# Kernel tuning notes

Hardware: AMD Instinct MI355X
Metric: run time of the kernel (lower is better)

Reference implementation:

```python
import jax, jax.numpy as jnp
import numpy as np

MARGIN = 0.3


def _l2norm(x, axis=-1):
    return x / (jnp.linalg.norm(x, axis=axis, keepdims=True) + 1e-12)


def setup_inputs() -> dict:
    key = jax.random.key(0)
    k1, k2, k3, k4 = jax.random.split(key, 4)
    n, P, d = 1024, 8, 2048
    global_feat = jax.random.normal(k1, (n, d), dtype=jnp.float32)
    partial_feat = jax.random.normal(k2, (n, P, d), dtype=jnp.float32)
    part_labels = jax.random.randint(k3, (n, P), 0, 2).astype(jnp.float32)
    global_labels = jax.random.randint(k4, (n,), 0, 64).astype(jnp.int64)
    return {"global_feat": global_feat, "partial_feat": partial_feat,
            "part_labels": part_labels, "global_labels": global_labels}


def reference(global_feat, partial_feat, part_labels, global_labels):
    # --- compute_distance (VGTripletLoss) ---
    g = _l2norm(global_feat)            # [n, d]
    p = _l2norm(partial_feat)           # [n, P, d]
    gs = (1.0 - g @ g.T) / 2.0          # [n, n]
    overlap = part_labels[:, None, :] * part_labels[None, :, :]   # [n, n, P]
    # per-part cosine distance: [n, n, P]
    slf = (1.0 - jnp.einsum('ipd,jpd->ijp', p, p)) / 2.0
    slf = slf * overlap
    dist = (slf.sum(-1) + gs) / (overlap.sum(-1) + 1.0)            # [n, n]

    # --- compute_loss: hard positive/negative mining ---
    mask = global_labels[:, None] == global_labels[None, :]        # [n, n]
    neg_inf = jnp.float32(-1e30)
    pos_inf = jnp.float32(1e30)
    dist_ap = jnp.max(jnp.where(mask, dist, neg_inf), axis=1)      # hardest positive
    dist_an = jnp.min(jnp.where(mask, pos_inf, dist), axis=1)      # hardest negative
    # MarginRankingLoss(y=1, reduction='mean'): max(0, dist_ap - dist_an + margin)
    loss = jnp.mean(jax.nn.relu(dist_ap - dist_an + MARGIN))
    return loss
```

## Files before the change

### kernel.cpp

```cpp
#include <hip/hip_runtime.h>

#define N 1024
#define D 2048
#define P 8
#define F 9
#define KTOT (F * D)
#define BM 128
#define BKT 32
#define MARGIN 0.3f

typedef float f32x4 __attribute__((ext_vector_type(4)));
typedef short s16x8 __attribute__((ext_vector_type(8)));

#define GLOBAL_AS __attribute__((address_space(1)))
#define LDS_AS __attribute__((address_space(3)))

__device__ __forceinline__ const float* feat_row(const float* __restrict__ g,
                                                 const float* __restrict__ p,
                                                 int i, int f) {
    return (f == 0) ? (g + (size_t)i * D)
                    : (p + ((size_t)i * P + (f - 1)) * D);
}

__device__ __forceinline__ unsigned f2bf(float x) {
    unsigned u = __float_as_uint(x);
    return (u + 0x7fffu + ((u >> 16) & 1u)) >> 16;
}

__global__ __launch_bounds__(256)
void pack_kernel(const float* __restrict__ gfeat,
                 const float* __restrict__ pfeat,
                 const float* __restrict__ plab,
                 unsigned short* __restrict__ V) {
    const int wid = (blockIdx.x << 2) | (threadIdx.x >> 6);
    const int lane = threadIdx.x & 63;
    const int i = wid / F, f = wid % F;
    const float* src = feat_row(gfeat, pfeat, i, f);
    const float4* s4 = (const float4*)src;
    float4 a[4][2];
    #pragma unroll
    for (int q = 0; q < 4; ++q) {
        a[q][0] = s4[(q * 64 + lane) * 2];
        a[q][1] = s4[(q * 64 + lane) * 2 + 1];
    }
    float ss = 0.f;
    #pragma unroll
    for (int q = 0; q < 4; ++q)
        #pragma unroll
        for (int h = 0; h < 2; ++h)
            ss += a[q][h].x * a[q][h].x + a[q][h].y * a[q][h].y
                + a[q][h].z * a[q][h].z + a[q][h].w * a[q][h].w;
    #pragma unroll
    for (int m = 32; m > 0; m >>= 1) ss += __shfl_xor(ss, m, 64);
    const float ls = (f == 0) ? 1.0f : plab[i * P + (f - 1)];
    const float inv = ls / (sqrtf(ss) + 1e-12f);
    unsigned short* dst = V + (size_t)wid * D;
    #pragma unroll
    for (int q = 0; q < 4; ++q) {
        uint4 o;
        o.x = f2bf(a[q][0].x * inv) | (f2bf(a[q][0].y * inv) << 16);
        o.y = f2bf(a[q][0].z * inv) | (f2bf(a[q][0].w * inv) << 16);
        o.z = f2bf(a[q][1].x * inv) | (f2bf(a[q][1].y * inv) << 16);
        o.w = f2bf(a[q][1].z * inv) | (f2bf(a[q][1].w * inv) << 16);
        *(uint4*)&dst[(size_t)(q * 64 + lane) * 8] = o;
    }
}

__global__ __launch_bounds__(256)
void gemm_kernel(const unsigned short* __restrict__ V,
                 float* __restrict__ part, int ks) {
    __shared__ short As[2][BM * BKT];
    __shared__ short Bs[2][BM * BKT];

    const int nwg = gridDim.x * gridDim.y;
    const int l = blockIdx.x + gridDim.x * blockIdx.y;
    const int q = nwg >> 3;
    const int wg = (l & 7) * q + (l >> 3);
    const int t36 = wg % 36;
    const int bz = wg / 36;

    int by = 0, rem = t36;
    while (rem >= 8 - by) { rem -= 8 - by; ++by; }
    const int bx = by + rem;

    const int t = threadIdx.x;
    const int wave = t >> 6, lane = t & 63;
    const int i0 = by * BM;
    const int j0 = bx * BM;
    const int kbase = bz * ks;
    const int nsteps = ks >> 5;

    const unsigned short* Ap = V + (size_t)(i0 + (t >> 2)) * KTOT + kbase + (t & 3) * 8;
    const unsigned short* Bp = V + (size_t)(j0 + (t >> 2)) * KTOT + kbase + (t & 3) * 8;

    const int kq = lane >> 4;
    const int aoff = ((wave & 1) * 64 + (lane & 15)) * BKT + kq * 8;
    const int boff = ((wave >> 1) * 64 + (lane & 15)) * BKT + kq * 8;

    f32x4 acc[4][4];
    #pragma unroll
    for (int m = 0; m < 4; ++m)
        #pragma unroll
        for (int n = 0; n < 4; ++n)
            acc[m][n] = (f32x4){0.f, 0.f, 0.f, 0.f};

#define STAGE(b) do {                                                          \
    __builtin_amdgcn_global_load_lds((const GLOBAL_AS void*)Ap,                \
        (LDS_AS void*)(&As[(b)][0] + t * 8), 16, 0, 0);                        \
    __builtin_amdgcn_global_load_lds((const GLOBAL_AS void*)(Ap + (size_t)64 * KTOT), \
        (LDS_AS void*)(&As[(b)][2048] + t * 8), 16, 0, 0);                     \
    __builtin_amdgcn_global_load_lds((const GLOBAL_AS void*)Bp,                \
        (LDS_AS void*)(&Bs[(b)][0] + t * 8), 16, 0, 0);                        \
    __builtin_amdgcn_global_load_lds((const GLOBAL_AS void*)(Bp + (size_t)64 * KTOT), \
        (LDS_AS void*)(&Bs[(b)][2048] + t * 8), 16, 0, 0);                     \
    Ap += BKT; Bp += BKT;                                                      \
} while (0)

#define COMPUTE(b) do {                                                        \
    s16x8 af[4], bf[4];                                                        \
    _Pragma("unroll")                                                          \
    for (int m = 0; m < 4; ++m)                                                \
        af[m] = *(const s16x8*)(&As[(b)][aoff + m * 16 * BKT]);                \
    _Pragma("unroll")                                                          \
    for (int n = 0; n < 4; ++n)                                                \
        bf[n] = *(const s16x8*)(&Bs[(b)][boff + n * 16 * BKT]);                \
    _Pragma("unroll")                                                          \
    for (int m = 0; m < 4; ++m)                                                \
        _Pragma("unroll")                                                      \
        for (int n = 0; n < 4; ++n)                                            \
            acc[m][n] = __builtin_amdgcn_mfma_f32_16x16x32_bf16(               \
                af[m], bf[n], acc[m][n], 0, 0, 0);                             \
} while (0)

    STAGE(0);
    __syncthreads();

    int cur = 0;
    for (int ksi = 0; ksi < nsteps - 1; ++ksi) {
        STAGE(cur ^ 1);
        COMPUTE(cur);
        __syncthreads();
        cur ^= 1;
    }
    COMPUTE(cur);

#undef STAGE
#undef COMPUTE

    float* outp = part + (size_t)bz * N * N;
    const int rbase = i0 + (wave & 1) * 64 + (lane >> 4) * 4;
    const int cbase = j0 + (wave >> 1) * 64 + (lane & 15);
    #pragma unroll
    for (int m = 0; m < 4; ++m)
        #pragma unroll
        for (int n = 0; n < 4; ++n)
            #pragma unroll
            for (int r = 0; r < 4; ++r)
                outp[(size_t)(rbase + m * 16 + r) * N + cbase + n * 16] = acc[m][n][r];

    if (bx != by) {
        #pragma unroll
        for (int m = 0; m < 4; ++m)
            #pragma unroll
            for (int n = 0; n < 4; ++n)
                #pragma unroll
                for (int r = 0; r < 4; ++r)
                    outp[(size_t)(cbase + n * 16) * N + rbase + m * 16 + r] = acc[m][n][r];
    }
}

template <int S>
__global__ __launch_bounds__(256)
void mine_kernel(const float* __restrict__ part,
                 const float* __restrict__ plab,
                 const int* __restrict__ glab,
                 float* __restrict__ rowloss) {
    const int i = blockIdx.x;
    const int t = threadIdx.x;
    const int wave = t >> 6, lane = t & 63;
    const int j = t * 4;

    float4 dot = {0.f, 0.f, 0.f, 0.f};
    #pragma unroll
    for (int s = 0; s < S; ++s) {
        float4 v = *(const float4*)&part[(size_t)s * N * N + (size_t)i * N + j];
        dot.x += v.x; dot.y += v.y; dot.z += v.z; dot.w += v.w;
    }

    float labj[4][8];
    const float4* pj = (const float4*)&plab[(size_t)j * P];
    #pragma unroll
    for (int q = 0; q < 8; ++q) ((float4*)labj)[q] = pj[q];
    int4 gj = *(const int4*)&glab[j];

    const int li = glab[i];
    float lab_i[P];
    #pragma unroll
    for (int c = 0; c < P; ++c) lab_i[c] = plab[i * P + c];

    float ap = -1e30f, an = 1e30f;
    const float dv[4] = {dot.x, dot.y, dot.z, dot.w};
    const int gv[4] = {gj.x, gj.y, gj.z, gj.w};
    #pragma unroll
    for (int u = 0; u < 4; ++u) {
        float ov = 0.f;
        #pragma unroll
        for (int c = 0; c < P; ++c) ov += lab_i[c] * labj[u][c];
        float d = 0.5f - dv[u] / (2.0f * (ov + 1.0f));
        if (gv[u] == li) ap = fmaxf(ap, d);
        else             an = fminf(an, d);
    }

    #pragma unroll
    for (int m = 32; m > 0; m >>= 1) {
        ap = fmaxf(ap, __shfl_xor(ap, m, 64));
        an = fminf(an, __shfl_xor(an, m, 64));
    }
    __shared__ float sap[4], san[4];
    if (lane == 0) { sap[wave] = ap; san[wave] = an; }
    __syncthreads();
    if (t == 0) {
        float A = fmaxf(fmaxf(sap[0], sap[1]), fmaxf(sap[2], sap[3]));
        float B = fminf(fminf(san[0], san[1]), fminf(san[2], san[3]));
        rowloss[i] = fmaxf(0.f, A - B + MARGIN);
    }
}

__global__ void reduce_kernel(const float* __restrict__ rowloss,
                              float* __restrict__ out) {
    const int t = threadIdx.x;
    float s = rowloss[t] + rowloss[t + 256] + rowloss[t + 512] + rowloss[t + 768];
    __shared__ float red[256];
    red[t] = s;
    __syncthreads();
    for (int st = 128; st > 0; st >>= 1) {
        if (t < st) red[t] += red[t + st];
        __syncthreads();
    }
    if (t == 0) out[0] = red[0] * (1.0f / N);
}

extern "C" void kernel_launch(void* const* d_in, const int* in_sizes, int n_in,
                              void* d_out, int out_size, void* d_ws, size_t ws_size,
                              hipStream_t stream) {
    const float* gfeat = (const float*)d_in[0];
    const float* pfeat = (const float*)d_in[1];
    const float* plab  = (const float*)d_in[2];
    const int*   glab  = (const int*)d_in[3];
    float* out = (float*)d_out;

    const size_t vbytes = (size_t)N * KTOT * 2;
    const size_t slice  = (size_t)N * N * 4;

    int S = (ws_size != 0 && ws_size >= vbytes + 16 * slice + 4096) ? 16 : 8;
    const int ks = KTOT / S;

    char* ws = (char*)d_ws;
    unsigned short* V = (unsigned short*)ws;
    float* part    = (float*)(ws + vbytes);
    float* rowloss = (float*)(ws + vbytes + (size_t)S * slice);

    pack_kernel<<<N * F / 4, 256, 0, stream>>>(gfeat, pfeat, plab, V);
    gemm_kernel<<<dim3(36, S), 256, 0, stream>>>(V, part, ks);
    if (S == 16)
        mine_kernel<16><<<N, 256, 0, stream>>>(part, plab, glab, rowloss);
    else
        mine_kernel<8><<<N, 256, 0, stream>>>(part, plab, glab, rowloss);
    reduce_kernel<<<1, 256, 0, stream>>>(rowloss, out);
}
```

Before: 164.4 us.

## Double GEMM K-tile with XOR-swizzled LDS layout and batch rows in mining kernel

The GEMM K-step grows from 32 to 64 bf16 elements, halving the number of barrier-separated iterations. The global-to-LDS staging is reorganised so each wave loads 8-row groups into an XOR-swizzled layout, and fragment reads apply the same swizzle to avoid LDS bank conflicts on the wider rows. LDS use per buffer doubles. The mining kernel now handles four rows per block, reusing the column-label loads and launching a quarter as many blocks, at the cost of extra barriers per row.

After: 170.7 us. 1.04x slower.

```diff
diff --git a/kernel.cpp b/kernel.cpp
--- a/kernel.cpp
+++ b/kernel.cpp
@@ -6,7 +6,7 @@
 #define F 9
 #define KTOT (F * D)
 #define BM 128
-#define BKT 32
+#define BKT 64
 #define MARGIN 0.3f
 
 typedef float f32x4 __attribute__((ext_vector_type(4)));
@@ -88,14 +88,19 @@
     const int i0 = by * BM;
     const int j0 = bx * BM;
     const int kbase = bz * ks;
-    const int nsteps = ks >> 5;
-
-    const unsigned short* Ap = V + (size_t)(i0 + (t >> 2)) * KTOT + kbase + (t & 3) * 8;
-    const unsigned short* Bp = V + (size_t)(j0 + (t >> 2)) * KTOT + kbase + (t & 3) * 8;
+    const int nsteps = ks >> 6;
+
+    const int sg = lane >> 3;
+    const int sc = lane & 7;
+    const int rl0 = wave * 32 + sg;
+    const unsigned short* Ag = V + (size_t)(i0 + rl0) * KTOT + kbase + ((sc ^ sg) << 3);
+    const unsigned short* Bg = V + (size_t)(j0 + rl0) * KTOT + kbase + ((sc ^ sg) << 3);
+    const int ldsoff = wave * 2048 + sg * 64 + sc * 8;
 
     const int kq = lane >> 4;
-    const int aoff = ((wave & 1) * 64 + (lane & 15)) * BKT + kq * 8;
-    const int boff = ((wave >> 1) * 64 + (lane & 15)) * BKT + kq * 8;
+    const int r7 = lane & 7;
+    const int arow0 = (wave & 1) * 64 + (lane & 15);
+    const int brow0 = (wave >> 1) * 64 + (lane & 15);
 
     f32x4 acc[4][4];
     #pragma unroll
@@ -105,31 +110,39 @@
             acc[m][n] = (f32x4){0.f, 0.f, 0.f, 0.f};
 
 #define STAGE(b) do {                                                          \
-    __builtin_amdgcn_global_load_lds((const GLOBAL_AS void*)Ap,                \
-        (LDS_AS void*)(&As[(b)][0] + t * 8), 16, 0, 0);                        \
-    __builtin_amdgcn_global_load_lds((const GLOBAL_AS void*)(Ap + (size_t)64 * KTOT), \
-        (LDS_AS void*)(&As[(b)][2048] + t * 8), 16, 0, 0);                     \
-    __builtin_amdgcn_global_load_lds((const GLOBAL_AS void*)Bp,                \
-        (LDS_AS void*)(&Bs[(b)][0] + t * 8), 16, 0, 0);                        \
-    __builtin_amdgcn_global_load_lds((const GLOBAL_AS void*)(Bp + (size_t)64 * KTOT), \
-        (LDS_AS void*)(&Bs[(b)][2048] + t * 8), 16, 0, 0);                     \
-    Ap += BKT; Bp += BKT;                                                      \
+    _Pragma("unroll")                                                          \
+    for (int c = 0; c < 4; ++c) {                                              \
+        __builtin_amdgcn_global_load_lds(                                      \
+            (const GLOBAL_AS void*)(Ag + (size_t)(c * 8) * KTOT),              \
+            (LDS_AS void*)(&As[(b)][ldsoff + c * 512]), 16, 0, 0);             \
+        __builtin_amdgcn_global_load_lds(                                      \
+            (const GLOBAL_AS void*)(Bg + (size_t)(c * 8) * KTOT),              \
+            (LDS_AS void*)(&Bs[(b)][ldsoff + c * 512]), 16, 0, 0);             \
+    }                                                                          \
+    Ag += BKT; Bg += BKT;                                                      \
 } while (0)
 
 #define COMPUTE(b) do {                                                        \
-    s16x8 af[4], bf[4];                                                        \
     _Pragma("unroll")                                                          \
-    for (int m = 0; m < 4; ++m)                                                \
-        af[m] = *(const s16x8*)(&As[(b)][aoff + m * 16 * BKT]);                \
-    _Pragma("unroll")                                                          \
-    for (int n = 0; n < 4; ++n)                                                \
-        bf[n] = *(const s16x8*)(&Bs[(b)][boff + n * 16 * BKT]);                \
-    _Pragma("unroll")                                                          \
-    for (int m = 0; m < 4; ++m)                                                \
+    for (int ks2 = 0; ks2 < 2; ++ks2) {                                        \
+        s16x8 af[4], bf[4];                                                    \
         _Pragma("unroll")                                                      \
-        for (int n = 0; n < 4; ++n)                                            \
-            acc[m][n] = __builtin_amdgcn_mfma_f32_16x16x32_bf16(               \
-                af[m], bf[n], acc[m][n], 0, 0, 0);                             \
+        for (int m = 0; m < 4; ++m) {                                          \
+            const int R = arow0 + m * 16;                                      \
+            af[m] = *(const s16x8*)(&As[(b)][R * 64 + (((ks2 * 4 + kq) ^ r7) * 8)]); \
+        }                                                                      \
+        _Pragma("unroll")                                                      \
+        for (int n = 0; n < 4; ++n) {                                          \
+            const int R = brow0 + n * 16;                                      \
+            bf[n] = *(const s16x8*)(&Bs[(b)][R * 64 + (((ks2 * 4 + kq) ^ r7) * 8)]); \
+        }                                                                      \
+        _Pragma("unroll")                                                      \
+        for (int m = 0; m < 4; ++m)                                            \
+            _Pragma("unroll")                                                  \
+            for (int n = 0; n < 4; ++n)                                        \
+                acc[m][n] = __builtin_amdgcn_mfma_f32_16x16x32_bf16(           \
+                    af[m], bf[n], acc[m][n], 0, 0, 0);                         \
+    }                                                                          \
 } while (0)
 
     STAGE(0);
@@ -175,54 +188,61 @@
                  const float* __restrict__ plab,
                  const int* __restrict__ glab,
                  float* __restrict__ rowloss) {
-    const int i = blockIdx.x;
+    const int i0 = blockIdx.x * 4;
     const int t = threadIdx.x;
     const int wave = t >> 6, lane = t & 63;
     const int j = t * 4;
 
-    float4 dot = {0.f, 0.f, 0.f, 0.f};
-    #pragma unroll
-    for (int s = 0; s < S; ++s) {
-        float4 v = *(const float4*)&part[(size_t)s * N * N + (size_t)i * N + j];
-        dot.x += v.x; dot.y += v.y; dot.z += v.z; dot.w += v.w;
-    }
-
     float labj[4][8];
     const float4* pj = (const float4*)&plab[(size_t)j * P];
     #pragma unroll
-    for (int q = 0; q < 8; ++q) ((float4*)labj)[q] = pj[q];
-    int4 gj = *(const int4*)&glab[j];
-
-    const int li = glab[i];
-    float lab_i[P];
-    #pragma unroll
-    for (int c = 0; c < P; ++c) lab_i[c] = plab[i * P + c];
-
-    float ap = -1e30f, an = 1e30f;
-    const float dv[4] = {dot.x, dot.y, dot.z, dot.w};
+    for (int qq = 0; qq < 8; ++qq) ((float4*)labj)[qq] = pj[qq];
+    const int4 gj = *(const int4*)&glab[j];
     const int gv[4] = {gj.x, gj.y, gj.z, gj.w};
-    #pragma unroll
-    for (int u = 0; u < 4; ++u) {
-        float ov = 0.f;
-        #pragma unroll
-        for (int c = 0; c < P; ++c) ov += lab_i[c] * labj[u][c];
-        float d = 0.5f - dv[u] / (2.0f * (ov + 1.0f));
-        if (gv[u] == li) ap = fmaxf(ap, d);
-        else             an = fminf(an, d);
-    }
-
-    #pragma unroll
-    for (int m = 32; m > 0; m >>= 1) {
-        ap = fmaxf(ap, __shfl_xor(ap, m, 64));
-        an = fminf(an, __shfl_xor(an, m, 64));
-    }
+
     __shared__ float sap[4], san[4];
-    if (lane == 0) { sap[wave] = ap; san[wave] = an; }
-    __syncthreads();
-    if (t == 0) {
-        float A = fmaxf(fmaxf(sap[0], sap[1]), fmaxf(sap[2], sap[3]));
-        float B = fminf(fminf(san[0], san[1]), fminf(san[2], san[3]));
-        rowloss[i] = fmaxf(0.f, A - B + MARGIN);
+
+    #pragma unroll
+    for (int ri = 0; ri < 4; ++ri) {
+        const int i = i0 + ri;
+
+        float4 dot = {0.f, 0.f, 0.f, 0.f};
+        #pragma unroll
+        for (int s = 0; s < S; ++s) {
+            float4 v = *(const float4*)&part[(size_t)s * N * N + (size_t)i * N + j];
+            dot.x += v.x; dot.y += v.y; dot.z += v.z; dot.w += v.w;
+        }
+
+        const int li = glab[i];
+        float lab_i[P];
+        #pragma unroll
+        for (int c = 0; c < P; ++c) lab_i[c] = plab[i * P + c];
+
+        float ap = -1e30f, an = 1e30f;
+        const float dv[4] = {dot.x, dot.y, dot.z, dot.w};
+        #pragma unroll
+        for (int u = 0; u < 4; ++u) {
+            float ov = 0.f;
+            #pragma unroll
+            for (int c = 0; c < P; ++c) ov += lab_i[c] * labj[u][c];
+            float d = 0.5f - dv[u] / (2.0f * (ov + 1.0f));
+            if (gv[u] == li) ap = fmaxf(ap, d);
+            else             an = fminf(an, d);
+        }
+
+        #pragma unroll
+        for (int m = 32; m > 0; m >>= 1) {
+            ap = fmaxf(ap, __shfl_xor(ap, m, 64));
+            an = fminf(an, __shfl_xor(an, m, 64));
+        }
+        if (lane == 0) { sap[wave] = ap; san[wave] = an; }
+        __syncthreads();
+        if (t == 0) {
+            float A = fmaxf(fmaxf(sap[0], sap[1]), fmaxf(sap[2], sap[3]));
+            float B = fminf(fminf(san[0], san[1]), fminf(san[2], san[3]));
+            rowloss[i] = fmaxf(0.f, A - B + MARGIN);
+        }
+        __syncthreads();
     }
 }
 
@@ -263,8 +283,8 @@
     pack_kernel<<<N * F / 4, 256, 0, stream>>>(gfeat, pfeat, plab, V);
     gemm_kernel<<<dim3(36, S), 256, 0, stream>>>(V, part, ks);
     if (S == 16)
-        mine_kernel<16><<<N, 256, 0, stream>>>(part, plab, glab, rowloss);
+        mine_kernel<16><<<N / 4, 256, 0, stream>>>(part, plab, glab, rowloss);
     else
-        mine_kernel<8><<<N, 256, 0, stream>>>(part, plab, glab, rowloss);
+        mine_kernel<8><<<N / 4, 256, 0, stream>>>(part, plab, glab, rowloss);
     reduce_kernel<<<1, 256, 0, stream>>>(rowloss, out);
 }
```

## Swizzle GEMM LDS layout, relax barriers with vmcnt waits, batch mining rows

Applied to the files above, without the earlier changes.

Applies an XOR swizzle to the k-chunk placement in LDS for both the staging writes and the MFMA fragment reads, to cut LDS bank conflicts. It also replaces __syncthreads with explicit s_waitcnt vmcnt plus s_barrier, so the next tile's async loads can stay in flight while the current tile computes. The mining kernel now handles 4 rows per block to reuse the column labels and cut the block count, at the cost of extra barriers per row. The hand-written waitcnt counts are fragile if the compiler reorders or adds memory operations.

Measured after the change: 164.1 us. Within noise of the previous version (-0.2%).

```diff
diff --git a/kernel.cpp b/kernel.cpp
--- a/kernel.cpp
+++ b/kernel.cpp
@@ -90,12 +90,16 @@
     const int kbase = bz * ks;
     const int nsteps = ks >> 5;
 
-    const unsigned short* Ap = V + (size_t)(i0 + (t >> 2)) * KTOT + kbase + (t & 3) * 8;
-    const unsigned short* Bp = V + (size_t)(j0 + (t >> 2)) * KTOT + kbase + (t & 3) * 8;
+    const int srow = t >> 2;
+    const int schunk = (t & 3) ^ ((t >> 3) & 3);
+    const unsigned short* Ag = V + (size_t)(i0 + srow) * KTOT + kbase + schunk * 8;
+    const unsigned short* Bg = V + (size_t)(j0 + srow) * KTOT + kbase + schunk * 8;
 
     const int kq = lane >> 4;
-    const int aoff = ((wave & 1) * 64 + (lane & 15)) * BKT + kq * 8;
-    const int boff = ((wave >> 1) * 64 + (lane & 15)) * BKT + kq * 8;
+    const int rsw = ((lane & 15) >> 1) & 3;
+    const int kk = (kq ^ rsw) * 8;
+    const int arow0 = (wave & 1) * 64 + (lane & 15);
+    const int brow0 = (wave >> 1) * 64 + (lane & 15);
 
     f32x4 acc[4][4];
     #pragma unroll
@@ -105,25 +109,25 @@
             acc[m][n] = (f32x4){0.f, 0.f, 0.f, 0.f};
 
 #define STAGE(b) do {                                                          \
-    __builtin_amdgcn_global_load_lds((const GLOBAL_AS void*)Ap,                \
-        (LDS_AS void*)(&As[(b)][0] + t * 8), 16, 0, 0);                        \
-    __builtin_amdgcn_global_load_lds((const GLOBAL_AS void*)(Ap + (size_t)64 * KTOT), \
-        (LDS_AS void*)(&As[(b)][2048] + t * 8), 16, 0, 0);                     \
-    __builtin_amdgcn_global_load_lds((const GLOBAL_AS void*)Bp,                \
-        (LDS_AS void*)(&Bs[(b)][0] + t * 8), 16, 0, 0);                        \
-    __builtin_amdgcn_global_load_lds((const GLOBAL_AS void*)(Bp + (size_t)64 * KTOT), \
-        (LDS_AS void*)(&Bs[(b)][2048] + t * 8), 16, 0, 0);                     \
-    Ap += BKT; Bp += BKT;                                                      \
+    __builtin_amdgcn_global_load_lds((const GLOBAL_AS void*)Ag,                \
+        (LDS_AS void*)(&As[(b)][t * 8]), 16, 0, 0);                            \
+    __builtin_amdgcn_global_load_lds((const GLOBAL_AS void*)(Ag + (size_t)64 * KTOT), \
+        (LDS_AS void*)(&As[(b)][2048 + t * 8]), 16, 0, 0);                     \
+    __builtin_amdgcn_global_load_lds((const GLOBAL_AS void*)Bg,                \
+        (LDS_AS void*)(&Bs[(b)][t * 8]), 16, 0, 0);                            \
+    __builtin_amdgcn_global_load_lds((const GLOBAL_AS void*)(Bg + (size_t)64 * KTOT), \
+        (LDS_AS void*)(&Bs[(b)][2048 + t * 8]), 16, 0, 0);                     \
+    Ag += BKT; Bg += BKT;                                                      \
 } while (0)
 
 #define COMPUTE(b) do {                                                        \
     s16x8 af[4], bf[4];                                                        \
     _Pragma("unroll")                                                          \
     for (int m = 0; m < 4; ++m)                                                \
-        af[m] = *(const s16x8*)(&As[(b)][aoff + m * 16 * BKT]);                \
+        af[m] = *(const s16x8*)(&As[(b)][(arow0 + m * 16) * 32 + kk]);         \
     _Pragma("unroll")                                                          \
     for (int n = 0; n < 4; ++n)                                                \
-        bf[n] = *(const s16x8*)(&Bs[(b)][boff + n * 16 * BKT]);                \
+        bf[n] = *(const s16x8*)(&Bs[(b)][(brow0 + n * 16) * 32 + kk]);         \
     _Pragma("unroll")                                                          \
     for (int m = 0; m < 4; ++m)                                                \
         _Pragma("unroll")                                                      \
@@ -133,15 +137,18 @@
 } while (0)
 
     STAGE(0);
-    __syncthreads();
 
     int cur = 0;
     for (int ksi = 0; ksi < nsteps - 1; ++ksi) {
         STAGE(cur ^ 1);
+        asm volatile("s_waitcnt vmcnt(4)" ::: "memory");
+        __builtin_amdgcn_s_barrier();
         COMPUTE(cur);
-        __syncthreads();
+        __builtin_amdgcn_s_barrier();
         cur ^= 1;
     }
+    asm volatile("s_waitcnt vmcnt(0)" ::: "memory");
+    __builtin_amdgcn_s_barrier();
     COMPUTE(cur);
 
 #undef STAGE
@@ -175,54 +182,61 @@
                  const float* __restrict__ plab,
                  const int* __restrict__ glab,
                  float* __restrict__ rowloss) {
-    const int i = blockIdx.x;
+    const int i0 = blockIdx.x * 4;
     const int t = threadIdx.x;
     const int wave = t >> 6, lane = t & 63;
     const int j = t * 4;
 
-    float4 dot = {0.f, 0.f, 0.f, 0.f};
-    #pragma unroll
-    for (int s = 0; s < S; ++s) {
-        float4 v = *(const float4*)&part[(size_t)s * N * N + (size_t)i * N + j];
-        dot.x += v.x; dot.y += v.y; dot.z += v.z; dot.w += v.w;
-    }
-
     float labj[4][8];
     const float4* pj = (const float4*)&plab[(size_t)j * P];
     #pragma unroll
-    for (int q = 0; q < 8; ++q) ((float4*)labj)[q] = pj[q];
-    int4 gj = *(const int4*)&glab[j];
-
-    const int li = glab[i];
-    float lab_i[P];
-    #pragma unroll
-    for (int c = 0; c < P; ++c) lab_i[c] = plab[i * P + c];
-
-    float ap = -1e30f, an = 1e30f;
-    const float dv[4] = {dot.x, dot.y, dot.z, dot.w};
+    for (int qq = 0; qq < 8; ++qq) ((float4*)labj)[qq] = pj[qq];
+    const int4 gj = *(const int4*)&glab[j];
     const int gv[4] = {gj.x, gj.y, gj.z, gj.w};
-    #pragma unroll
-    for (int u = 0; u < 4; ++u) {
-        float ov = 0.f;
-        #pragma unroll
-        for (int c = 0; c < P; ++c) ov += lab_i[c] * labj[u][c];
-        float d = 0.5f - dv[u] / (2.0f * (ov + 1.0f));
-        if (gv[u] == li) ap = fmaxf(ap, d);
-        else             an = fminf(an, d);
-    }
-
-    #pragma unroll
-    for (int m = 32; m > 0; m >>= 1) {
-        ap = fmaxf(ap, __shfl_xor(ap, m, 64));
-        an = fminf(an, __shfl_xor(an, m, 64));
-    }
+
     __shared__ float sap[4], san[4];
-    if (lane == 0) { sap[wave] = ap; san[wave] = an; }
-    __syncthreads();
-    if (t == 0) {
-        float A = fmaxf(fmaxf(sap[0], sap[1]), fmaxf(sap[2], sap[3]));
-        float B = fminf(fminf(san[0], san[1]), fminf(san[2], san[3]));
-        rowloss[i] = fmaxf(0.f, A - B + MARGIN);
+
+    #pragma unroll
+    for (int ri = 0; ri < 4; ++ri) {
+        const int i = i0 + ri;
+
+        float4 dot = {0.f, 0.f, 0.f, 0.f};
+        #pragma unroll
+        for (int s = 0; s < S; ++s) {
+            float4 v = *(const float4*)&part[(size_t)s * N * N + (size_t)i * N + j];
+            dot.x += v.x; dot.y += v.y; dot.z += v.z; dot.w += v.w;
+        }
+
+        const int li = glab[i];
+        float lab_i[P];
+        #pragma unroll
+        for (int c = 0; c < P; ++c) lab_i[c] = plab[i * P + c];
+
+        float ap = -1e30f, an = 1e30f;
+        const float dv[4] = {dot.x, dot.y, dot.z, dot.w};
+        #pragma unroll
+        for (int u = 0; u < 4; ++u) {
+            float ov = 0.f;
+            #pragma unroll
+            for (int c = 0; c < P; ++c) ov += lab_i[c] * labj[u][c];
+            float d = 0.5f - dv[u] / (2.0f * (ov + 1.0f));
+            if (gv[u] == li) ap = fmaxf(ap, d);
+            else             an = fminf(an, d);
+        }
+
+        #pragma unroll
+        for (int m = 32; m > 0; m >>= 1) {
+            ap = fmaxf(ap, __shfl_xor(ap, m, 64));
+            an = fminf(an, __shfl_xor(an, m, 64));
+        }
+        if (lane == 0) { sap[wave] = ap; san[wave] = an; }
+        __syncthreads();
+        if (t == 0) {
+            float A = fmaxf(fmaxf(sap[0], sap[1]), fmaxf(sap[2], sap[3]));
+            float B = fminf(fminf(san[0], san[1]), fminf(san[2], san[3]));
+            rowloss[i] = fmaxf(0.f, A - B + MARGIN);
+        }
+        __syncthreads();
     }
 }
 
@@ -263,8 +277,8 @@
     pack_kernel<<<N * F / 4, 256, 0, stream>>>(gfeat, pfeat, plab, V);
     gemm_kernel<<<dim3(36, S), 256, 0, stream>>>(V, part, ks);
     if (S == 16)
-        mine_kernel<16><<<N, 256, 0, stream>>>(part, plab, glab, rowloss);
+        mine_kernel<16><<<N / 4, 256, 0, stream>>>(part, plab, glab, rowloss);
     else
-        mine_kernel<8><<<N, 256, 0, stream>>>(part, plab, glab, rowloss);
+        mine_kernel<8><<<N / 4, 256, 0, stream>>>(part, plab, glab, rowloss);
     reduce_kernel<<<1, 256, 0, stream>>>(rowloss, out);
 }
```
